# Performance work log

Measured on AMD Instinct MI355X. Metric: run time of the kernel, lower is better.

## Reference

```python
import jax, jax.numpy as jnp
import numpy as np

B_SZ, N_IN, N_CTX, UNITS, RANK = 4096, 4096, 512, 4096, 256


def setup_inputs() -> dict:
    key = jax.random.key(0)
    ks = jax.random.split(key, 8)
    inputs = jax.random.normal(ks[0], (B_SZ, N_IN), dtype=jnp.float32)
    context = jax.random.normal(ks[1], (B_SZ, N_CTX), dtype=jnp.float32)
    # Orthogonal-ish init approximated by scaled normals (math-equivalent shapes)
    U = jax.random.normal(ks[2], (N_IN, RANK), dtype=jnp.float32) / np.sqrt(N_IN)
    S = jax.random.uniform(ks[3], (RANK,), dtype=jnp.float32, minval=0.5, maxval=1.5)
    V = jax.random.normal(ks[4], (UNITS, RANK), dtype=jnp.float32) / np.sqrt(UNITS)
    W = jax.random.normal(ks[5], (N_CTX, RANK), dtype=jnp.float32) / np.sqrt(N_CTX)
    B = jnp.zeros((RANK,), dtype=jnp.float32)
    bias = jnp.zeros((UNITS,), dtype=jnp.float32)
    return {"inputs": inputs, "context": context, "U": U, "S": S, "V": V, "W": W, "B": B, "bias": bias}


def reference(inputs, context, U, S, V, W, B, bias):
    # chi[b,r] = sigmoid(context @ W + B)
    chi = jax.nn.sigmoid(context @ W + B)                  # [B, R]
    # Original: kernel[b,n,m] = sum_r U[n,r]*S[r]*chi[b,r]*V[m,r];
    # out[b,m] = sum_n x[b,n]*kernel[b,n,m]. Algebraically equal to:
    t = (inputs @ U) * (S * chi)                           # [B, R]
    out = t @ V.T + bias                                   # first '+ self.bias'
    out = out + bias                                       # 'outputs += self.bias' (use_bias=True)
    return jax.nn.relu(out)
```

## Files before the change

### kernel.cpp

```cpp
#include <hip/hip_runtime.h>

#define B_SZ 4096
#define N_IN 4096
#define N_CTX 512
#define UNITS 4096
#define RANK 256
#define ZSPLIT 8

typedef __attribute__((ext_vector_type(8))) __bf16 bf16x8;
typedef __attribute__((ext_vector_type(4))) float f32x4;
typedef __attribute__((ext_vector_type(8))) unsigned short ushort8;
typedef __attribute__((ext_vector_type(4))) unsigned short ushort4v;

__device__ __forceinline__ unsigned short f2bf(float f) {
    unsigned int u = __float_as_uint(f);
    u += 0x7FFFu + ((u >> 16) & 1u);
    return (unsigned short)(u >> 16);
}
__device__ __forceinline__ float bf2f(unsigned short h) {
    return __uint_as_float(((unsigned int)h) << 16);
}
__device__ __forceinline__ void gload_lds16(const unsigned short* g, unsigned short* l) {
    __builtin_amdgcn_global_load_lds(
        (const __attribute__((address_space(1))) unsigned int*)g,
        (__attribute__((address_space(3))) unsigned int*)l, 16, 0, 0);
}
__device__ __forceinline__ bf16x8 ldfrag(const unsigned short* p) {
    ushort8 t = *(const ushort8*)p;
    return __builtin_bit_cast(bf16x8, t);
}

__global__ void prep(const float* __restrict__ U, const float* __restrict__ W,
                     const float* __restrict__ V,
                     unsigned short* __restrict__ UT, unsigned short* __restrict__ WT,
                     unsigned short* __restrict__ Vb) {
    __shared__ unsigned short t[64][66];
    int bid = blockIdx.x, tid = threadIdx.x;
    if (bid < 288) {
        const float* src; unsigned short* dst; int R, C, rb, cb;
        if (bid < 256) { src = U; dst = UT; R = N_IN; C = RANK; rb = (bid & 63) * 64; cb = (bid >> 6) * 64; }
        else { int b = bid - 256; src = W; dst = WT; R = N_CTX; C = RANK; rb = (b & 7) * 64; cb = (b >> 3) * 64; }
        int r = tid >> 4, c4 = (tid & 15) * 4;
        for (int i = 0; i < 4; i++) {
            float4 v = *(const float4*)(src + (size_t)(rb + r + i * 16) * C + cb + c4);
            t[r + i * 16][c4 + 0] = f2bf(v.x);
            t[r + i * 16][c4 + 1] = f2bf(v.y);
            t[r + i * 16][c4 + 2] = f2bf(v.z);
            t[r + i * 16][c4 + 3] = f2bf(v.w);
        }
        __syncthreads();
        int c = tid >> 3, r8 = (tid & 7) * 8;
        for (int j = 0; j < 2; j++) {
            int cc = c + j * 32;
            ushort8 o;
            for (int k = 0; k < 8; k++) o[k] = t[r8 + k][cc];
            *(ushort8*)(dst + (size_t)(cb + cc) * R + rb + r8) = o;
        }
    } else {
        size_t base = (size_t)(bid - 288) * 2048 + (size_t)tid * 8;
        float4 a = *(const float4*)(V + base);
        float4 b = *(const float4*)(V + base + 4);
        ushort8 o = { f2bf(a.x), f2bf(a.y), f2bf(a.z), f2bf(a.w),
                      f2bf(b.x), f2bf(b.y), f2bf(b.z), f2bf(b.w) };
        *(ushort8*)(Vb + base) = o;
    }
}


__launch_bounds__(256, 4)
__global__ void k1_chi(const float* __restrict__ ctx, const unsigned short* __restrict__ WT,
                       const float* __restrict__ S, const float* __restrict__ Bb,
                       unsigned short* __restrict__ Schi) {
    __shared__ unsigned short As[32 * 64];
    __shared__ unsigned short Bs[64 * 64];
    int tid = threadIdx.x, w = tid >> 6, lane = tid & 63;
    int ln15 = lane & 15, quad = lane >> 4;
    int wr = w >> 1, wc = w & 1;
    int tm = blockIdx.y * 32, tn = blockIdx.x * 64;
    f32x4 acc2[2] = {};
    int arow = tid >> 3, acs = tid & 7;
    const float* ag = ctx + (size_t)(tm + arow) * N_CTX + acs * 8;
    unsigned short* al = As + arow * 64 + (acs ^ (arow & 7)) * 8;
    int bl8 = lane >> 3, bcs = lane & 7;
    int bgc = (bcs ^ bl8) * 8;
    for (int kt = 0; kt < 8; kt++) {
        int k0 = kt * 64;
        for (int c = 0; c < 2; c++) {
            int row = w * 16 + c * 8 + bl8;
            gload_lds16(WT + (size_t)(tn + row) * N_CTX + k0 + bgc, Bs + row * 64 + bcs * 8);
        }
        {
            float4 v0 = *(const float4*)(ag + k0);
            float4 v1 = *(const float4*)(ag + k0 + 4);
            ushort8 a8 = { f2bf(v0.x), f2bf(v0.y), f2bf(v0.z), f2bf(v0.w),
                           f2bf(v1.x), f2bf(v1.y), f2bf(v1.z), f2bf(v1.w) };
            *(ushort8*)al = a8;
        }
        __syncthreads();
        for (int kh = 0; kh < 2; kh++) {
            int ch = kh * 4 + quad;
            bf16x8 af = ldfrag(As + (wr * 16 + ln15) * 64 + (ch ^ (ln15 & 7)) * 8);
            for (int j = 0; j < 2; j++) {
                int row = wc * 32 + j * 16 + ln15;
                bf16x8 bfr = ldfrag(Bs + row * 64 + (ch ^ (ln15 & 7)) * 8);
                acc2[j] = __builtin_amdgcn_mfma_f32_16x16x32_bf16(af, bfr, acc2[j], 0, 0, 0);
            }
        }
        __syncthreads();
    }
    for (int j = 0; j < 2; j++) {
        int col = tn + wc * 32 + j * 16 + ln15;
        float sv = S[col], bv = Bb[col];
        for (int r = 0; r < 4; r++) {
            int row = tm + wr * 16 + quad * 4 + r;
            float x = acc2[j][r] + bv;
            float chi = sv / (1.f + __expf(-x));
            Schi[(size_t)row * RANK + col] = f2bf(chi);
        }
    }
}

__launch_bounds__(256, 4)
__global__ void k2_t0(const float* __restrict__ X, const unsigned short* __restrict__ UT,
                      unsigned short* __restrict__ T0p) {
    __shared__ unsigned short As[64 * 64];
    __shared__ unsigned short Bs[128 * 64];
    int tid = threadIdx.x, w = tid >> 6, lane = tid & 63;
    int ln15 = lane & 15, quad = lane >> 4;
    int wr = w >> 1, wc = w & 1;
    int tm = blockIdx.y * 64, tn = blockIdx.x * 128;
    int kbase = blockIdx.z * (N_IN / ZSPLIT);
    f32x4 acc[2][4] = {};
    int arow = tid >> 2, acs0 = tid & 3;
    const float* ag = X + (size_t)(tm + arow) * N_IN + kbase;
    unsigned short* al0 = As + arow * 64 + ((acs0 + 0) ^ (arow & 7)) * 8;
    unsigned short* al1 = As + arow * 64 + ((acs0 + 4) ^ (arow & 7)) * 8;
    int bl8 = lane >> 3, bcs = lane & 7;
    int bgc = (bcs ^ bl8) * 8;
    for (int kt = 0; kt < (N_IN / ZSPLIT) / 64; kt++) {
        int k0 = kt * 64;
        for (int c = 0; c < 4; c++) {
            int row = w * 32 + c * 8 + bl8;
            gload_lds16(UT + (size_t)(tn + row) * N_IN + kbase + k0 + bgc, Bs + row * 64 + bcs * 8);
        }
        {
            float4 v0 = *(const float4*)(ag + k0 + acs0 * 8);
            float4 v1 = *(const float4*)(ag + k0 + acs0 * 8 + 4);
            float4 u0 = *(const float4*)(ag + k0 + (acs0 + 4) * 8);
            float4 u1 = *(const float4*)(ag + k0 + (acs0 + 4) * 8 + 4);
            ushort8 a8 = { f2bf(v0.x), f2bf(v0.y), f2bf(v0.z), f2bf(v0.w),
                           f2bf(v1.x), f2bf(v1.y), f2bf(v1.z), f2bf(v1.w) };
            ushort8 b8 = { f2bf(u0.x), f2bf(u0.y), f2bf(u0.z), f2bf(u0.w),
                           f2bf(u1.x), f2bf(u1.y), f2bf(u1.z), f2bf(u1.w) };
            *(ushort8*)al0 = a8;
            *(ushort8*)al1 = b8;
        }
        __syncthreads();
        for (int kh = 0; kh < 2; kh++) {
            int ch = kh * 4 + quad;
            int sw = (ch ^ (ln15 & 7)) * 8;
            bf16x8 af[2], bfr[4];
            for (int i = 0; i < 2; i++)
                af[i] = ldfrag(As + (wr * 32 + i * 16 + ln15) * 64 + sw);
            for (int j = 0; j < 4; j++)
                bfr[j] = ldfrag(Bs + (wc * 64 + j * 16 + ln15) * 64 + sw);
            for (int i = 0; i < 2; i++)
                for (int j = 0; j < 4; j++)
                    acc[i][j] = __builtin_amdgcn_mfma_f32_16x16x32_bf16(af[i], bfr[j], acc[i][j], 0, 0, 0);
        }
        __syncthreads();
    }
    unsigned short* P = T0p + (size_t)blockIdx.z * B_SZ * RANK;
    for (int i = 0; i < 2; i++)
        for (int j = 0; j < 4; j++) {
            int col = tn + wc * 64 + j * 16 + ln15;
            for (int r = 0; r < 4; r++) {
                int row = tm + wr * 32 + i * 16 + quad * 4 + r;
                P[(size_t)row * RANK + col] = f2bf(acc[i][j][r]);
            }
        }
}

__global__ void e_red(const unsigned short* __restrict__ T0p, const unsigned short* __restrict__ Schi,
                      unsigned short* __restrict__ T) {
    int i = blockIdx.x * 256 + threadIdx.x;
    const size_t stride = (size_t)B_SZ * RANK;
    float a[8] = {};
    for (int z = 0; z < ZSPLIT; z++) {
        ushort8 p = *(const ushort8*)(T0p + z * stride + (size_t)i * 8);
        for (int k = 0; k < 8; k++) a[k] += bf2f(p[k]);
    }
    ushort8 s = *(const ushort8*)(Schi + (size_t)i * 8);
    ushort8 o;
    for (int k = 0; k < 8; k++) o[k] = f2bf(a[k] * bf2f(s[k]));
    *(ushort8*)(T + (size_t)i * 8) = o;
}

__launch_bounds__(256, 4)
__global__ void k3_out(const unsigned short* __restrict__ T, const unsigned short* __restrict__ Vb,
                       const float* __restrict__ bias, float* __restrict__ out) {
    __shared__ unsigned short As[64 * 64];
    __shared__ unsigned short Bs[128 * 64];
    int tid = threadIdx.x, w = tid >> 6, lane = tid & 63;
    int ln15 = lane & 15, quad = lane >> 4;
    int wr = w >> 1, wc = w & 1;
    int tn = blockIdx.x * 128, tm = blockIdx.y * 64;
    f32x4 acc[2][4] = {};
    int bl8 = lane >> 3, bcs = lane & 7;
    int bgc = (bcs ^ bl8) * 8;
    for (int kt = 0; kt < RANK / 64; kt++) {
        int k0 = kt * 64;
        for (int c = 0; c < 2; c++) {
            int row = w * 16 + c * 8 + bl8;
            gload_lds16(T + (size_t)(tm + row) * RANK + k0 + bgc, As + row * 64 + bcs * 8);
        }
        for (int c = 0; c < 4; c++) {
            int row = w * 32 + c * 8 + bl8;
            gload_lds16(Vb + (size_t)(tn + row) * RANK + k0 + bgc, Bs + row * 64 + bcs * 8);
        }
        __syncthreads();
        for (int kh = 0; kh < 2; kh++) {
            int ch = kh * 4 + quad;
            int sw = (ch ^ (ln15 & 7)) * 8;
            bf16x8 af[2], bfr[4];
            for (int i = 0; i < 2; i++)
                af[i] = ldfrag(As + (wr * 32 + i * 16 + ln15) * 64 + sw);
            for (int j = 0; j < 4; j++)
                bfr[j] = ldfrag(Bs + (wc * 64 + j * 16 + ln15) * 64 + sw);
            for (int i = 0; i < 2; i++)
                for (int j = 0; j < 4; j++)
                    acc[i][j] = __builtin_amdgcn_mfma_f32_16x16x32_bf16(af[i], bfr[j], acc[i][j], 0, 0, 0);
        }
        __syncthreads();
    }
    for (int j = 0; j < 4; j++) {
        int col = tn + wc * 64 + j * 16 + ln15;
        float bv = 2.f * bias[col];
        for (int i = 0; i < 2; i++)
            for (int r = 0; r < 4; r++) {
                int row = tm + wr * 32 + i * 16 + quad * 4 + r;
                float v = acc[i][j][r] + bv;
                out[(size_t)row * UNITS + col] = fmaxf(v, 0.f);
            }
    }
}

extern "C" void kernel_launch(void* const* d_in, const int* in_sizes, int n_in,
                              void* d_out, int out_size, void* d_ws, size_t ws_size,
                              hipStream_t stream) {
    (void)in_sizes; (void)n_in; (void)out_size; (void)ws_size;
    const float* inputs  = (const float*)d_in[0];
    const float* context = (const float*)d_in[1];
    const float* U       = (const float*)d_in[2];
    const float* S       = (const float*)d_in[3];
    const float* V       = (const float*)d_in[4];
    const float* W       = (const float*)d_in[5];
    const float* Bb      = (const float*)d_in[6];
    const float* bias    = (const float*)d_in[7];
    float* out = (float*)d_out;

    char* ws = (char*)d_ws;
    size_t o = 0;
    unsigned short* UT   = (unsigned short*)(ws + o); o += (size_t)RANK * N_IN * 2;
    unsigned short* WT   = (unsigned short*)(ws + o); o += (size_t)RANK * N_CTX * 2;
    unsigned short* Vb   = (unsigned short*)(ws + o); o += (size_t)UNITS * RANK * 2;
    unsigned short* Schi = (unsigned short*)(ws + o); o += (size_t)B_SZ * RANK * 2;
    unsigned short* T    = (unsigned short*)(ws + o); o += (size_t)B_SZ * RANK * 2;
    unsigned short* T0p  = (unsigned short*)(ws + o); o += (size_t)ZSPLIT * B_SZ * RANK * 2;

    prep<<<800, 256, 0, stream>>>(U, W, V, UT, WT, Vb);
    k2_t0<<<dim3(RANK / 128, B_SZ / 64, ZSPLIT), 256, 0, stream>>>(inputs, UT, T0p);
    k1_chi<<<dim3(RANK / 64, B_SZ / 32), 256, 0, stream>>>(context, WT, S, Bb, Schi);
    e_red<<<(B_SZ * RANK) / (256 * 8), 256, 0, stream>>>(T0p, Schi, T);
    k3_out<<<dim3(UNITS / 128, B_SZ / 64), 256, 0, stream>>>(T, Vb, bias, out);
}
```

Before: 177.2 us.

## Double-buffer LDS tiles in all three GEMM kernels to overlap loads with MFMA

Converts the chi, t0 and output GEMM kernels from single-buffered LDS tiles to ping-pong buffers. The next K-tile's global-to-LDS loads and fp32 register loads are issued before the current tile's MFMAs, which also drops one barrier per iteration. It adds s_setprio around the MFMA block and lowers launch bounds from 4 to 3 blocks per CU to fit the doubled LDS. The cost is higher LDS and register use, which lowers occupancy.

```diff
diff --git a/kernel.cpp b/kernel.cpp
--- a/kernel.cpp
+++ b/kernel.cpp
@@ -10,7 +10,6 @@
 typedef __attribute__((ext_vector_type(8))) __bf16 bf16x8;
 typedef __attribute__((ext_vector_type(4))) float f32x4;
 typedef __attribute__((ext_vector_type(8))) unsigned short ushort8;
-typedef __attribute__((ext_vector_type(4))) unsigned short ushort4v;
 
 __device__ __forceinline__ unsigned short f2bf(float f) {
     unsigned int u = __float_as_uint(f);
@@ -71,8 +70,8 @@
 __global__ void k1_chi(const float* __restrict__ ctx, const unsigned short* __restrict__ WT,
                        const float* __restrict__ S, const float* __restrict__ Bb,
                        unsigned short* __restrict__ Schi) {
-    __shared__ unsigned short As[32 * 64];
-    __shared__ unsigned short Bs[64 * 64];
+    __shared__ unsigned short As[2][32 * 64];
+    __shared__ unsigned short Bs[2][64 * 64];
     int tid = threadIdx.x, w = tid >> 6, lane = tid & 63;
     int ln15 = lane & 15, quad = lane >> 4;
     int wr = w >> 1, wc = w & 1;
@@ -80,33 +79,52 @@
     f32x4 acc2[2] = {};
     int arow = tid >> 3, acs = tid & 7;
     const float* ag = ctx + (size_t)(tm + arow) * N_CTX + acs * 8;
-    unsigned short* al = As + arow * 64 + (acs ^ (arow & 7)) * 8;
+    int aoff = arow * 64 + (acs ^ (arow & 7)) * 8;
     int bl8 = lane >> 3, bcs = lane & 7;
     int bgc = (bcs ^ bl8) * 8;
+
+#define K1_STAGE_B(buf, k0) do { \
+    for (int c = 0; c < 2; c++) { \
+        int row = w * 16 + c * 8 + bl8; \
+        gload_lds16(WT + (size_t)(tn + row) * N_CTX + (k0) + bgc, &Bs[buf][row * 64 + bcs * 8]); \
+    } } while (0)
+
+    K1_STAGE_B(0, 0);
+    {
+        float4 v0 = *(const float4*)(ag);
+        float4 v1 = *(const float4*)(ag + 4);
+        ushort8 a8 = { f2bf(v0.x), f2bf(v0.y), f2bf(v0.z), f2bf(v0.w),
+                       f2bf(v1.x), f2bf(v1.y), f2bf(v1.z), f2bf(v1.w) };
+        *(ushort8*)&As[0][aoff] = a8;
+    }
+    __syncthreads();
+
+    int cur = 0;
     for (int kt = 0; kt < 8; kt++) {
-        int k0 = kt * 64;
-        for (int c = 0; c < 2; c++) {
-            int row = w * 16 + c * 8 + bl8;
-            gload_lds16(WT + (size_t)(tn + row) * N_CTX + k0 + bgc, Bs + row * 64 + bcs * 8);
-        }
-        {
-            float4 v0 = *(const float4*)(ag + k0);
-            float4 v1 = *(const float4*)(ag + k0 + 4);
+        int nxt = cur ^ 1;
+        bool pf = (kt < 7);
+        float4 v0, v1;
+        if (pf) {
+            int k0 = (kt + 1) * 64;
+            K1_STAGE_B(nxt, k0);
+            v0 = *(const float4*)(ag + k0);
+            v1 = *(const float4*)(ag + k0 + 4);
+        }
+        for (int kh = 0; kh < 2; kh++) {
+            int ch = kh * 4 + quad;
+            bf16x8 af = ldfrag(&As[cur][(wr * 16 + ln15) * 64 + (ch ^ (ln15 & 7)) * 8]);
+            for (int j = 0; j < 2; j++) {
+                bf16x8 bfr = ldfrag(&Bs[cur][(wc * 32 + j * 16 + ln15) * 64 + (ch ^ (ln15 & 7)) * 8]);
+                acc2[j] = __builtin_amdgcn_mfma_f32_16x16x32_bf16(af, bfr, acc2[j], 0, 0, 0);
+            }
+        }
+        if (pf) {
             ushort8 a8 = { f2bf(v0.x), f2bf(v0.y), f2bf(v0.z), f2bf(v0.w),
                            f2bf(v1.x), f2bf(v1.y), f2bf(v1.z), f2bf(v1.w) };
-            *(ushort8*)al = a8;
+            *(ushort8*)&As[nxt][aoff] = a8;
         }
         __syncthreads();
-        for (int kh = 0; kh < 2; kh++) {
-            int ch = kh * 4 + quad;
-            bf16x8 af = ldfrag(As + (wr * 16 + ln15) * 64 + (ch ^ (ln15 & 7)) * 8);
-            for (int j = 0; j < 2; j++) {
-                int row = wc * 32 + j * 16 + ln15;
-                bf16x8 bfr = ldfrag(Bs + row * 64 + (ch ^ (ln15 & 7)) * 8);
-                acc2[j] = __builtin_amdgcn_mfma_f32_16x16x32_bf16(af, bfr, acc2[j], 0, 0, 0);
-            }
-        }
-        __syncthreads();
+        cur = nxt;
     }
     for (int j = 0; j < 2; j++) {
         int col = tn + wc * 32 + j * 16 + ln15;
@@ -118,13 +136,14 @@
             Schi[(size_t)row * RANK + col] = f2bf(chi);
         }
     }
-}
-
-__launch_bounds__(256, 4)
+#undef K1_STAGE_B
+}
+
+__launch_bounds__(256, 3)
 __global__ void k2_t0(const float* __restrict__ X, const unsigned short* __restrict__ UT,
                       unsigned short* __restrict__ T0p) {
-    __shared__ unsigned short As[64 * 64];
-    __shared__ unsigned short Bs[128 * 64];
+    __shared__ unsigned short As[2][64 * 64];
+    __shared__ unsigned short Bs[2][128 * 64];
     int tid = threadIdx.x, w = tid >> 6, lane = tid & 63;
     int ln15 = lane & 15, quad = lane >> 4;
     int wr = w >> 1, wc = w & 1;
@@ -133,42 +152,70 @@
     f32x4 acc[2][4] = {};
     int arow = tid >> 2, acs0 = tid & 3;
     const float* ag = X + (size_t)(tm + arow) * N_IN + kbase;
-    unsigned short* al0 = As + arow * 64 + ((acs0 + 0) ^ (arow & 7)) * 8;
-    unsigned short* al1 = As + arow * 64 + ((acs0 + 4) ^ (arow & 7)) * 8;
+    int aoff0 = arow * 64 + ((acs0 + 0) ^ (arow & 7)) * 8;
+    int aoff1 = arow * 64 + ((acs0 + 4) ^ (arow & 7)) * 8;
     int bl8 = lane >> 3, bcs = lane & 7;
     int bgc = (bcs ^ bl8) * 8;
-    for (int kt = 0; kt < (N_IN / ZSPLIT) / 64; kt++) {
-        int k0 = kt * 64;
-        for (int c = 0; c < 4; c++) {
-            int row = w * 32 + c * 8 + bl8;
-            gload_lds16(UT + (size_t)(tn + row) * N_IN + kbase + k0 + bgc, Bs + row * 64 + bcs * 8);
-        }
-        {
-            float4 v0 = *(const float4*)(ag + k0 + acs0 * 8);
-            float4 v1 = *(const float4*)(ag + k0 + acs0 * 8 + 4);
-            float4 u0 = *(const float4*)(ag + k0 + (acs0 + 4) * 8);
-            float4 u1 = *(const float4*)(ag + k0 + (acs0 + 4) * 8 + 4);
-            ushort8 a8 = { f2bf(v0.x), f2bf(v0.y), f2bf(v0.z), f2bf(v0.w),
-                           f2bf(v1.x), f2bf(v1.y), f2bf(v1.z), f2bf(v1.w) };
-            ushort8 b8 = { f2bf(u0.x), f2bf(u0.y), f2bf(u0.z), f2bf(u0.w),
-                           f2bf(u1.x), f2bf(u1.y), f2bf(u1.z), f2bf(u1.w) };
-            *(ushort8*)al0 = a8;
-            *(ushort8*)al1 = b8;
-        }
-        __syncthreads();
+    const int NT = (N_IN / ZSPLIT) / 64;
+
+#define K2_STAGE_B(buf, k0) do { \
+    for (int c = 0; c < 4; c++) { \
+        int row = w * 32 + c * 8 + bl8; \
+        gload_lds16(UT + (size_t)(tn + row) * N_IN + kbase + (k0) + bgc, &Bs[buf][row * 64 + bcs * 8]); \
+    } } while (0)
+
+    K2_STAGE_B(0, 0);
+    {
+        float4 v0 = *(const float4*)(ag + acs0 * 8);
+        float4 v1 = *(const float4*)(ag + acs0 * 8 + 4);
+        float4 u0 = *(const float4*)(ag + (acs0 + 4) * 8);
+        float4 u1 = *(const float4*)(ag + (acs0 + 4) * 8 + 4);
+        ushort8 a8 = { f2bf(v0.x), f2bf(v0.y), f2bf(v0.z), f2bf(v0.w),
+                       f2bf(v1.x), f2bf(v1.y), f2bf(v1.z), f2bf(v1.w) };
+        ushort8 b8 = { f2bf(u0.x), f2bf(u0.y), f2bf(u0.z), f2bf(u0.w),
+                       f2bf(u1.x), f2bf(u1.y), f2bf(u1.z), f2bf(u1.w) };
+        *(ushort8*)&As[0][aoff0] = a8;
+        *(ushort8*)&As[0][aoff1] = b8;
+    }
+    __syncthreads();
+
+    int cur = 0;
+    for (int kt = 0; kt < NT; kt++) {
+        int nxt = cur ^ 1;
+        bool pf = (kt < NT - 1);
+        float4 v0, v1, u0, u1;
+        if (pf) {
+            int k0 = (kt + 1) * 64;
+            K2_STAGE_B(nxt, k0);
+            v0 = *(const float4*)(ag + k0 + acs0 * 8);
+            v1 = *(const float4*)(ag + k0 + acs0 * 8 + 4);
+            u0 = *(const float4*)(ag + k0 + (acs0 + 4) * 8);
+            u1 = *(const float4*)(ag + k0 + (acs0 + 4) * 8 + 4);
+        }
+        __builtin_amdgcn_s_setprio(1);
         for (int kh = 0; kh < 2; kh++) {
             int ch = kh * 4 + quad;
             int sw = (ch ^ (ln15 & 7)) * 8;
             bf16x8 af[2], bfr[4];
             for (int i = 0; i < 2; i++)
-                af[i] = ldfrag(As + (wr * 32 + i * 16 + ln15) * 64 + sw);
+                af[i] = ldfrag(&As[cur][(wr * 32 + i * 16 + ln15) * 64 + sw]);
             for (int j = 0; j < 4; j++)
-                bfr[j] = ldfrag(Bs + (wc * 64 + j * 16 + ln15) * 64 + sw);
+                bfr[j] = ldfrag(&Bs[cur][(wc * 64 + j * 16 + ln15) * 64 + sw]);
             for (int i = 0; i < 2; i++)
                 for (int j = 0; j < 4; j++)
                     acc[i][j] = __builtin_amdgcn_mfma_f32_16x16x32_bf16(af[i], bfr[j], acc[i][j], 0, 0, 0);
         }
+        __builtin_amdgcn_s_setprio(0);
+        if (pf) {
+            ushort8 a8 = { f2bf(v0.x), f2bf(v0.y), f2bf(v0.z), f2bf(v0.w),
+                           f2bf(v1.x), f2bf(v1.y), f2bf(v1.z), f2bf(v1.w) };
+            ushort8 b8 = { f2bf(u0.x), f2bf(u0.y), f2bf(u0.z), f2bf(u0.w),
+                           f2bf(u1.x), f2bf(u1.y), f2bf(u1.z), f2bf(u1.w) };
+            *(ushort8*)&As[nxt][aoff0] = a8;
+            *(ushort8*)&As[nxt][aoff1] = b8;
+        }
         __syncthreads();
+        cur = nxt;
     }
     unsigned short* P = T0p + (size_t)blockIdx.z * B_SZ * RANK;
     for (int i = 0; i < 2; i++)
@@ -179,6 +226,7 @@
                 P[(size_t)row * RANK + col] = f2bf(acc[i][j][r]);
             }
         }
+#undef K2_STAGE_B
 }
 
 __global__ void e_red(const unsigned short* __restrict__ T0p, const unsigned short* __restrict__ Schi,
@@ -196,11 +244,11 @@
     *(ushort8*)(T + (size_t)i * 8) = o;
 }
 
-__launch_bounds__(256, 4)
+__launch_bounds__(256, 3)
 __global__ void k3_out(const unsigned short* __restrict__ T, const unsigned short* __restrict__ Vb,
                        const float* __restrict__ bias, float* __restrict__ out) {
-    __shared__ unsigned short As[64 * 64];
-    __shared__ unsigned short Bs[128 * 64];
+    __shared__ unsigned short As[2][64 * 64];
+    __shared__ unsigned short Bs[2][128 * 64];
     int tid = threadIdx.x, w = tid >> 6, lane = tid & 63;
     int ln15 = lane & 15, quad = lane >> 4;
     int wr = w >> 1, wc = w & 1;
@@ -208,30 +256,42 @@
     f32x4 acc[2][4] = {};
     int bl8 = lane >> 3, bcs = lane & 7;
     int bgc = (bcs ^ bl8) * 8;
+
+#define K3_STAGE(buf, k0) do { \
+    for (int c = 0; c < 2; c++) { \
+        int row = w * 16 + c * 8 + bl8; \
+        gload_lds16(T + (size_t)(tm + row) * RANK + (k0) + bgc, &As[buf][row * 64 + bcs * 8]); \
+    } \
+    for (int c = 0; c < 4; c++) { \
+        int row = w * 32 + c * 8 + bl8; \
+        gload_lds16(Vb + (size_t)(tn + row) * RANK + (k0) + bgc, &Bs[buf][row * 64 + bcs * 8]); \
+    } } while (0)
+
+    K3_STAGE(0, 0);
+    __syncthreads();
+
+    int cur = 0;
     for (int kt = 0; kt < RANK / 64; kt++) {
-        int k0 = kt * 64;
-        for (int c = 0; c < 2; c++) {
-            int row = w * 16 + c * 8 + bl8;
-            gload_lds16(T + (size_t)(tm + row) * RANK + k0 + bgc, As + row * 64 + bcs * 8);
-        }
-        for (int c = 0; c < 4; c++) {
-            int row = w * 32 + c * 8 + bl8;
-            gload_lds16(Vb + (size_t)(tn + row) * RANK + k0 + bgc, Bs + row * 64 + bcs * 8);
-        }
-        __syncthreads();
+        int nxt = cur ^ 1;
+        if (kt < RANK / 64 - 1) {
+            K3_STAGE(nxt, (kt + 1) * 64);
+        }
+        __builtin_amdgcn_s_setprio(1);
         for (int kh = 0; kh < 2; kh++) {
             int ch = kh * 4 + quad;
             int sw = (ch ^ (ln15 & 7)) * 8;
             bf16x8 af[2], bfr[4];
             for (int i = 0; i < 2; i++)
-                af[i] = ldfrag(As + (wr * 32 + i * 16 + ln15) * 64 + sw);
+                af[i] = ldfrag(&As[cur][(wr * 32 + i * 16 + ln15) * 64 + sw]);
             for (int j = 0; j < 4; j++)
-                bfr[j] = ldfrag(Bs + (wc * 64 + j * 16 + ln15) * 64 + sw);
+                bfr[j] = ldfrag(&Bs[cur][(wc * 64 + j * 16 + ln15) * 64 + sw]);
             for (int i = 0; i < 2; i++)
                 for (int j = 0; j < 4; j++)
                     acc[i][j] = __builtin_amdgcn_mfma_f32_16x16x32_bf16(af[i], bfr[j], acc[i][j], 0, 0, 0);
         }
+        __builtin_amdgcn_s_setprio(0);
         __syncthreads();
+        cur = nxt;
     }
     for (int j = 0; j < 4; j++) {
         int col = tn + wc * 64 + j * 16 + ln15;
@@ -243,6 +303,7 @@
                 out[(size_t)row * UNITS + col] = fmaxf(v, 0.f);
             }
     }
+#undef K3_STAGE
 }
 
 extern "C" void kernel_launch(void* const* d_in, const int* in_sizes, int n_in,
```

Measured after the change: 184.5 us. 1.04x slower.
